# Kernel tuning notes

Hardware: AMD Instinct MI355X
Metric: run time of the kernel (lower is better)

## Reference

```python
import jax, jax.numpy as jnp
import numpy as np

N_HEADS = 8
OUT_DIM = 256   # node_dim + time_dim
KEY_DIM = 384   # node_dim + edge_dim + time_dim
HEAD_DIM = OUT_DIM // N_HEADS
LN_EPS = 1e-5


def setup_inputs() -> dict:
    key = jax.random.key(0)
    ks = jax.random.split(key, 12)
    B, N, D = 8192, 32, 128
    s = lambda fan_in: 1.0 / np.sqrt(fan_in)
    return {
        "node_feat": jax.random.normal(ks[0], (B, D), jnp.float32),
        "time_feat": jax.random.normal(ks[1], (B, D), jnp.float32),
        "edge_feat": jax.random.normal(ks[2], (B, N, D), jnp.float32),
        "nbr_node_feat": jax.random.normal(ks[3], (B, N, D), jnp.float32),
        "nbr_time_feat": jax.random.normal(ks[4], (B, N, D), jnp.float32),
        "nbr_mask": jax.random.randint(ks[5], (B, N), 0, 2, jnp.int64),
        # parameters, stored as [in, out] so y = x @ W
        "W_Q": jax.random.uniform(ks[6], (OUT_DIM, OUT_DIM), jnp.float32, -s(OUT_DIM), s(OUT_DIM)),
        "W_KV": jax.random.uniform(ks[7], (KEY_DIM, 2 * OUT_DIM), jnp.float32, -s(KEY_DIM), s(KEY_DIM)),
        "W_O": jax.random.uniform(ks[8], (OUT_DIM, OUT_DIM), jnp.float32, -s(OUT_DIM), s(OUT_DIM)),
        "b_O": jax.random.uniform(ks[9], (OUT_DIM,), jnp.float32, -s(OUT_DIM), s(OUT_DIM)),
        "ln_gamma": jnp.ones((OUT_DIM,), jnp.float32),
        "ln_beta": jnp.zeros((OUT_DIM,), jnp.float32),
    }


def reference(node_feat, time_feat, edge_feat, nbr_node_feat, nbr_time_feat,
              nbr_mask, W_Q, W_KV, W_O, b_O, ln_gamma, ln_beta):
    B = node_feat.shape[0]
    # query/residual: [B, out_dim] (query length is 1)
    R = jnp.concatenate([node_feat, time_feat], axis=1)
    Q = (R @ W_Q).reshape(B, N_HEADS, HEAD_DIM)                    # [B,H,d]
    Z = jnp.concatenate([nbr_node_feat, edge_feat, nbr_time_feat], axis=-1) @ W_KV  # [B,N,2*out]
    K = Z[:, :, :OUT_DIM].reshape(B, -1, N_HEADS, HEAD_DIM)        # [B,N,H,d]
    V = Z[:, :, OUT_DIM:].reshape(B, -1, N_HEADS, HEAD_DIM)
    A = jnp.einsum("bhd,bnhd->bhn", Q, K) * (HEAD_DIM ** -0.5)    # [B,H,N]
    masked = (nbr_mask == 0)[:, None, :]                           # [B,1,N]
    A = jnp.where(masked, jnp.float32(-1e10), A)
    A = jax.nn.softmax(A, axis=-1)                                 # dropout is identity (eval / p used at inference off)
    O = jnp.einsum("bhn,bnhd->bhd", A, V).reshape(B, OUT_DIM)
    out = O @ W_O + b_O
    x = out + R
    mu = jnp.mean(x, axis=-1, keepdims=True)
    var = jnp.mean(jnp.square(x - mu), axis=-1, keepdims=True)
    return (x - mu) * jax.lax.rsqrt(var + LN_EPS) * ln_gamma + ln_beta
```

## Files before the change

### kernel.cpp

```cpp
#include <hip/hip_runtime.h>

typedef __attribute__((ext_vector_type(8))) short bf16x8;
typedef __attribute__((ext_vector_type(4))) float f32x4;

#define MSTRIDE 264
#define XSTRIDE 392

__device__ __align__(16) unsigned short g_WQT[256 * 256];
__device__ __align__(16) unsigned short g_WKVT[512 * 384];
__device__ __align__(16) unsigned short g_WOT[256 * 256];

__device__ __forceinline__ float b2f(unsigned short u) {
    union { unsigned int i; float f; } v; v.i = ((unsigned int)u) << 16; return v.f;
}
__device__ __forceinline__ unsigned short f2b(float f) {
    union { float f; unsigned int i; } v; v.f = f;
    unsigned int x = v.i;
    return (unsigned short)((x + 0x7fffu + ((x >> 16) & 1u)) >> 16);
}

__global__ void transcvt(const float* __restrict__ src, unsigned short* __restrict__ dst,
                         int R, int C) {
    __shared__ float tile[32][33];
    const int c0 = blockIdx.x * 32, r0 = blockIdx.y * 32;
    const int tx = threadIdx.x, ty = threadIdx.y;
#pragma unroll
    for (int i = 0; i < 32; i += 8)
        tile[ty + i][tx] = src[(size_t)(r0 + ty + i) * C + (c0 + tx)];
    __syncthreads();
#pragma unroll
    for (int i = 0; i < 32; i += 8)
        dst[(size_t)(c0 + ty + i) * R + (r0 + tx)] = f2b(tile[tx][ty + i]);
}

__device__ __forceinline__ void ld8f(const float* __restrict__ s, unsigned short* dst) {
    const float4 a = *(const float4*)s;
    const float4 b = *(const float4*)(s + 4);
    unsigned short t[8];
    t[0] = f2b(a.x); t[1] = f2b(a.y); t[2] = f2b(a.z); t[3] = f2b(a.w);
    t[4] = f2b(b.x); t[5] = f2b(b.y); t[6] = f2b(b.z); t[7] = f2b(b.w);
    *(uint4*)dst = *(const uint4*)t;
}

__global__ __launch_bounds__(256, 2) void ta_fused(
    const float* __restrict__ node,
    const float* __restrict__ timef,
    const float* __restrict__ edge,
    const float* __restrict__ nbrnode,
    const float* __restrict__ nbrtime,
    const int* __restrict__ nmask,
    const float* __restrict__ bO,
    const float* __restrict__ gam,
    const float* __restrict__ bet,
    float* __restrict__ out)
{
    __shared__ __align__(16) unsigned short Xs[64 * XSTRIDE];
    __shared__ __align__(16) unsigned short Rb[16 * MSTRIDE];
    __shared__ __align__(16) unsigned short Ob[16 * MSTRIDE];
    __shared__ float lnb[2][256];
    __shared__ int   mk[2][32];

    const int gb0  = blockIdx.x * 2;
    const int tid  = threadIdx.x;
    const int w    = tid >> 6;
    const int lane = tid & 63;
    const int l15  = lane & 15;
    const int quad = lane >> 4;

    bool m64 = true;
    for (int i = 1; i < 64; i += 2) m64 = m64 && (nmask[i] == 0);

    {
        unsigned int* pO = (unsigned int*)Ob;
        for (int i = tid; i < 16 * MSTRIDE / 2; i += 256) pO[i] = 0u;
        unsigned int* pR = (unsigned int*)Rb;
        for (int i = tid + MSTRIDE; i < 16 * MSTRIDE / 2; i += 256) pR[i] = 0u;
    }
    if (tid < 64) {
        const int b = tid >> 5, s = tid & 31;
        if (s < 16) ld8f(node  + (size_t)(gb0 + b) * 128 + s * 8,        &Rb[b * MSTRIDE + s * 8]);
        else        ld8f(timef + (size_t)(gb0 + b) * 128 + (s - 16) * 8, &Rb[b * MSTRIDE + s * 8]);
    } else if (tid < 128) {
        const int t = tid - 64, b = t >> 5, n = t & 31;
        const size_t j = (size_t)(gb0 + b) * 32 + n;
        mk[b][n] = m64 ? nmask[2 * j] : nmask[j];
    }
#pragma unroll
    for (int i = 0; i < 12; i++) {
        const int g  = i * 256 + tid;
        const int r  = g / 48, c8 = g % 48;
        const float* base; int koff;
        if (c8 < 16)      { base = nbrnode; koff = c8 * 8; }
        else if (c8 < 32) { base = edge;    koff = (c8 - 16) * 8; }
        else              { base = nbrtime; koff = (c8 - 32) * 8; }
        ld8f(base + (size_t)(gb0 * 32 + r) * 128 + koff, &Xs[r * XSTRIDE + c8 * 8]);
    }
    __syncthreads();

    const f32x4 zero4 = {0.0f, 0.0f, 0.0f, 0.0f};

    f32x4 accq[4];
#pragma unroll
    for (int ct = 0; ct < 4; ct++) accq[ct] = zero4;
    {
        const unsigned short* wq = g_WQT + (size_t)(w * 64 + l15) * 256 + quad * 8;
#pragma unroll 2
        for (int kc = 0; kc < 8; kc++) {
            const bf16x8 afr = *(const bf16x8*)(&Rb[l15 * MSTRIDE + kc * 32 + quad * 8]);
#pragma unroll
            for (int ct = 0; ct < 4; ct++) {
                const bf16x8 b = *(const bf16x8*)(wq + (size_t)(ct * 16) * 256 + kc * 32);
                accq[ct] = __builtin_amdgcn_mfma_f32_16x16x32_bf16(afr, b, accq[ct], 0, 0, 0);
            }
        }
    }

    f32x4 accK[4][4], accV[4][4];
#pragma unroll
    for (int rt = 0; rt < 4; rt++)
#pragma unroll
        for (int ct = 0; ct < 4; ct++) { accK[rt][ct] = zero4; accV[rt][ct] = zero4; }
    {
        const unsigned short* wkv = g_WKVT + (size_t)(w * 64 + l15) * 384 + quad * 8;
#pragma unroll 2
        for (int kc = 0; kc < 12; kc++) {
            bf16x8 af[4];
#pragma unroll
            for (int rt = 0; rt < 4; rt++)
                af[rt] = *(const bf16x8*)(&Xs[(rt * 16 + l15) * XSTRIDE + kc * 32 + quad * 8]);
            bf16x8 bK[4], bV[4];
#pragma unroll
            for (int ct = 0; ct < 4; ct++) {
                bK[ct] = *(const bf16x8*)(wkv + (size_t)(ct * 16) * 384 + kc * 32);
                bV[ct] = *(const bf16x8*)(wkv + (size_t)(256 + ct * 16) * 384 + kc * 32);
            }
            __builtin_amdgcn_s_setprio(1);
#pragma unroll
            for (int ct = 0; ct < 4; ct++)
#pragma unroll
                for (int rt = 0; rt < 4; rt++) {
                    accK[rt][ct] = __builtin_amdgcn_mfma_f32_16x16x32_bf16(af[rt], bK[ct], accK[rt][ct], 0, 0, 0);
                    accV[rt][ct] = __builtin_amdgcn_mfma_f32_16x16x32_bf16(af[rt], bV[ct], accV[rt][ct], 0, 0, 0);
                }
            __builtin_amdgcn_s_setprio(0);
        }
    }

    float aw[2][2][2][4];
    const float scl = 0.17677669529663687f;
#pragma unroll
    for (int bb = 0; bb < 2; bb++) {
        float qv[4];
#pragma unroll
        for (int ct = 0; ct < 4; ct++) qv[ct] = __shfl(accq[ct][bb], l15, 64);
#pragma unroll
        for (int hl = 0; hl < 2; hl++) {
            float sv[2][4];
#pragma unroll
            for (int rtl = 0; rtl < 2; rtl++) {
                const int rt = bb * 2 + rtl;
#pragma unroll
                for (int rg = 0; rg < 4; rg++)
                    sv[rtl][rg] = accK[rt][2 * hl][rg] * qv[2 * hl]
                                + accK[rt][2 * hl + 1][rg] * qv[2 * hl + 1];
            }
#pragma unroll
            for (int m = 1; m <= 8; m <<= 1)
#pragma unroll
                for (int rtl = 0; rtl < 2; rtl++)
#pragma unroll
                    for (int rg = 0; rg < 4; rg++)
                        sv[rtl][rg] += __shfl_xor(sv[rtl][rg], m, 64);
            float mx = -3.0e38f;
#pragma unroll
            for (int rtl = 0; rtl < 2; rtl++)
#pragma unroll
                for (int rg = 0; rg < 4; rg++) {
                    const int n = rtl * 16 + quad * 4 + rg;
                    sv[rtl][rg] = (mk[bb][n] != 0) ? sv[rtl][rg] * scl : -1.0e10f;
                    mx = fmaxf(mx, sv[rtl][rg]);
                }
            mx = fmaxf(mx, __shfl_xor(mx, 16, 64));
            mx = fmaxf(mx, __shfl_xor(mx, 32, 64));
            float sum = 0.0f;
#pragma unroll
            for (int rtl = 0; rtl < 2; rtl++)
#pragma unroll
                for (int rg = 0; rg < 4; rg++) {
                    const float e = __expf(sv[rtl][rg] - mx);
                    aw[bb][hl][rtl][rg] = e;
                    sum += e;
                }
            sum += __shfl_xor(sum, 16, 64);
            sum += __shfl_xor(sum, 32, 64);
            const float inv = 1.0f / sum;
#pragma unroll
            for (int rtl = 0; rtl < 2; rtl++)
#pragma unroll
                for (int rg = 0; rg < 4; rg++)
                    aw[bb][hl][rtl][rg] *= inv;
        }
    }

#pragma unroll
    for (int bb = 0; bb < 2; bb++)
#pragma unroll
        for (int hl = 0; hl < 2; hl++)
#pragma unroll
            for (int ctl = 0; ctl < 2; ctl++) {
                const int ct = hl * 2 + ctl;
                float o = 0.0f;
#pragma unroll
                for (int rtl = 0; rtl < 2; rtl++)
#pragma unroll
                    for (int rg = 0; rg < 4; rg++)
                        o += aw[bb][hl][rtl][rg] * accV[bb * 2 + rtl][ct][rg];
                o += __shfl_xor(o, 16, 64);
                o += __shfl_xor(o, 32, 64);
                if (quad == 0) {
                    const int col = (w * 2 + hl) * 32 + ctl * 16 + l15;
                    Ob[bb * MSTRIDE + col] = f2b(o);
                }
            }
    __syncthreads();

    f32x4 acco[4];
#pragma unroll
    for (int ct = 0; ct < 4; ct++) acco[ct] = zero4;
    {
        const unsigned short* wo = g_WOT + (size_t)(w * 64 + l15) * 256 + quad * 8;
#pragma unroll 2
        for (int kc = 0; kc < 8; kc++) {
            const bf16x8 afr = *(const bf16x8*)(&Ob[l15 * MSTRIDE + kc * 32 + quad * 8]);
#pragma unroll
            for (int ct = 0; ct < 4; ct++) {
                const bf16x8 b = *(const bf16x8*)(wo + (size_t)(ct * 16) * 256 + kc * 32);
                acco[ct] = __builtin_amdgcn_mfma_f32_16x16x32_bf16(afr, b, acco[ct], 0, 0, 0);
            }
        }
    }
    if (quad == 0) {
#pragma unroll
        for (int ct = 0; ct < 4; ct++) {
#pragma unroll
            for (int r = 0; r < 2; r++) {
                const int col = w * 64 + ct * 16 + l15;
                lnb[r][col] = acco[ct][r] + bO[col] + b2f(Rb[r * MSTRIDE + col]);
            }
        }
    }
    __syncthreads();

    if (w < 2) {
        const int bb = w;
        float x[4]; float s = 0.0f;
#pragma unroll
        for (int i = 0; i < 4; i++) { x[i] = lnb[bb][lane + i * 64]; s += x[i]; }
#pragma unroll
        for (int m = 1; m <= 32; m <<= 1) s += __shfl_xor(s, m, 64);
        const float mu = s * (1.0f / 256.0f);
        float s2 = 0.0f;
#pragma unroll
        for (int i = 0; i < 4; i++) { const float d = x[i] - mu; s2 += d * d; }
#pragma unroll
        for (int m = 1; m <= 32; m <<= 1) s2 += __shfl_xor(s2, m, 64);
        const float rstd = rsqrtf(s2 * (1.0f / 256.0f) + 1e-5f);
#pragma unroll
        for (int i = 0; i < 4; i++) {
            const int col = lane + i * 64;
            out[(size_t)(gb0 + bb) * 256 + col] =
                (x[i] - mu) * rstd * gam[col] + bet[col];
        }
    }
}

extern "C" void kernel_launch(void* const* d_in, const int* in_sizes, int n_in,
                              void* d_out, int out_size, void* d_ws, size_t ws_size,
                              hipStream_t stream) {
    const float* node    = (const float*)d_in[0];
    const float* timef   = (const float*)d_in[1];
    const float* edge    = (const float*)d_in[2];
    const float* nbrnode = (const float*)d_in[3];
    const float* nbrtime = (const float*)d_in[4];
    const int*   nmask   = (const int*)d_in[5];
    const float* W_Q     = (const float*)d_in[6];
    const float* W_KV    = (const float*)d_in[7];
    const float* W_O     = (const float*)d_in[8];
    const float* bO      = (const float*)d_in[9];
    const float* gam     = (const float*)d_in[10];
    const float* bet     = (const float*)d_in[11];

    unsigned short *wqt, *wkvt, *wot;
    hipGetSymbolAddress((void**)&wqt,  HIP_SYMBOL(g_WQT));
    hipGetSymbolAddress((void**)&wkvt, HIP_SYMBOL(g_WKVT));
    hipGetSymbolAddress((void**)&wot,  HIP_SYMBOL(g_WOT));

    transcvt<<<dim3(8, 8),   dim3(32, 8), 0, stream>>>(W_Q,  wqt,  256, 256);
    transcvt<<<dim3(16, 12), dim3(32, 8), 0, stream>>>(W_KV, wkvt, 384, 512);
    transcvt<<<dim3(8, 8),   dim3(32, 8), 0, stream>>>(W_O,  wot,  256, 256);

    ta_fused<<<4096, 256, 0, stream>>>(node, timef, edge, nbrnode, nbrtime, nmask,
                                       bO, gam, bet, (float*)d_out);
}
```

Measured before the change: 682.2 us.

## Software-pipeline weight and activation loads in fused attention GEMMs, merge weight conversion

Each GEMM loop (Q, KV, O projections) now double-buffers its weight and LDS fragments, prefetching the next k-chunk while MFMAs run, and the first weight fragments are issued before the barrier. Q values go to shared memory instead of being kept live through the KV loop, and the mask check uses an OR reduction. The three weight transpose-convert launches are merged into one. Register pressure rises from the extra buffers under launch_bounds(256,2), which could cause spills.

```diff
diff --git a/kernel.cpp b/kernel.cpp
--- a/kernel.cpp
+++ b/kernel.cpp
@@ -19,10 +19,17 @@
     return (unsigned short)((x + 0x7fffu + ((x >> 16) & 1u)) >> 16);
 }
 
-__global__ void transcvt(const float* __restrict__ src, unsigned short* __restrict__ dst,
-                         int R, int C) {
+__global__ void transcvt_all(const float* __restrict__ wq, const float* __restrict__ wkv,
+                             const float* __restrict__ wo,
+                             unsigned short* __restrict__ dq, unsigned short* __restrict__ dkv,
+                             unsigned short* __restrict__ dwo) {
     __shared__ float tile[32][33];
-    const int c0 = blockIdx.x * 32, r0 = blockIdx.y * 32;
+    const int b = blockIdx.x;
+    const float* src; unsigned short* dst; int R, C, bx, by;
+    if (b < 64)       { src = wq;  dst = dq;  R = 256; C = 256; bx = b & 7;  by = b >> 3; }
+    else if (b < 256) { const int t = b - 64;  src = wkv; dst = dkv; R = 384; C = 512; bx = t & 15; by = t >> 4; }
+    else              { const int t = b - 256; src = wo;  dst = dwo; R = 256; C = 256; bx = t & 7;  by = t >> 3; }
+    const int c0 = bx * 32, r0 = by * 32;
     const int tx = threadIdx.x, ty = threadIdx.y;
 #pragma unroll
     for (int i = 0; i < 32; i += 8)
@@ -57,6 +64,7 @@
     __shared__ __align__(16) unsigned short Xs[64 * XSTRIDE];
     __shared__ __align__(16) unsigned short Rb[16 * MSTRIDE];
     __shared__ __align__(16) unsigned short Ob[16 * MSTRIDE];
+    __shared__ float Qs[2][256];
     __shared__ float lnb[2][256];
     __shared__ int   mk[2][32];
 
@@ -67,8 +75,10 @@
     const int l15  = lane & 15;
     const int quad = lane >> 4;
 
-    bool m64 = true;
-    for (int i = 1; i < 64; i += 2) m64 = m64 && (nmask[i] == 0);
+    int orv = 0;
+#pragma unroll
+    for (int i = 1; i < 64; i += 2) orv |= nmask[i];
+    const bool m64 = (orv == 0);
 
     {
         unsigned int* pO = (unsigned int*)Ob;
@@ -95,6 +105,22 @@
         else              { base = nbrtime; koff = (c8 - 32) * 8; }
         ld8f(base + (size_t)(gb0 * 32 + r) * 128 + koff, &Xs[r * XSTRIDE + c8 * 8]);
     }
+
+    const unsigned short* wq  = g_WQT  + (size_t)(w * 64 + l15) * 256 + quad * 8;
+    const unsigned short* wkv = g_WKVT + (size_t)(w * 64 + l15) * 384 + quad * 8;
+    const unsigned short* wo  = g_WOT  + (size_t)(w * 64 + l15) * 256 + quad * 8;
+    bf16x8 bq[2][4], bK[2][4], bV[2][4];
+#pragma unroll
+    for (int p = 0; p < 2; p++)
+#pragma unroll
+        for (int ct = 0; ct < 4; ct++)
+            bq[p][ct] = *(const bf16x8*)(wq + (size_t)(ct * 16) * 256 + p * 32);
+#pragma unroll
+    for (int ct = 0; ct < 4; ct++) {
+        bK[0][ct] = *(const bf16x8*)(wkv + (size_t)(ct * 16) * 384);
+        bV[0][ct] = *(const bf16x8*)(wkv + (size_t)(256 + ct * 16) * 384);
+    }
+
     __syncthreads();
 
     const f32x4 zero4 = {0.0f, 0.0f, 0.0f, 0.0f};
@@ -103,15 +129,28 @@
 #pragma unroll
     for (int ct = 0; ct < 4; ct++) accq[ct] = zero4;
     {
-        const unsigned short* wq = g_WQT + (size_t)(w * 64 + l15) * 256 + quad * 8;
-#pragma unroll 2
+        bf16x8 aq[2];
+        aq[0] = *(const bf16x8*)(&Rb[l15 * MSTRIDE + 0 * 32 + quad * 8]);
+        aq[1] = *(const bf16x8*)(&Rb[l15 * MSTRIDE + 1 * 32 + quad * 8]);
+#pragma unroll
         for (int kc = 0; kc < 8; kc++) {
-            const bf16x8 afr = *(const bf16x8*)(&Rb[l15 * MSTRIDE + kc * 32 + quad * 8]);
-#pragma unroll
-            for (int ct = 0; ct < 4; ct++) {
-                const bf16x8 b = *(const bf16x8*)(wq + (size_t)(ct * 16) * 256 + kc * 32);
-                accq[ct] = __builtin_amdgcn_mfma_f32_16x16x32_bf16(afr, b, accq[ct], 0, 0, 0);
-            }
+            const int s = kc & 1;
+#pragma unroll
+            for (int ct = 0; ct < 4; ct++)
+                accq[ct] = __builtin_amdgcn_mfma_f32_16x16x32_bf16(aq[s], bq[s][ct], accq[ct], 0, 0, 0);
+            if (kc + 2 < 8) {
+                aq[s] = *(const bf16x8*)(&Rb[l15 * MSTRIDE + (kc + 2) * 32 + quad * 8]);
+#pragma unroll
+                for (int ct = 0; ct < 4; ct++)
+                    bq[s][ct] = *(const bf16x8*)(wq + (size_t)(ct * 16) * 256 + (kc + 2) * 32);
+            }
+        }
+    }
+    if (quad == 0) {
+#pragma unroll
+        for (int ct = 0; ct < 4; ct++) {
+            Qs[0][w * 64 + ct * 16 + l15] = accq[ct][0];
+            Qs[1][w * 64 + ct * 16 + l15] = accq[ct][1];
         }
     }
 
@@ -121,30 +160,48 @@
 #pragma unroll
         for (int ct = 0; ct < 4; ct++) { accK[rt][ct] = zero4; accV[rt][ct] = zero4; }
     {
-        const unsigned short* wkv = g_WKVT + (size_t)(w * 64 + l15) * 384 + quad * 8;
-#pragma unroll 2
+        bf16x8 af[2][4];
+#pragma unroll
+        for (int rt = 0; rt < 4; rt++)
+            af[0][rt] = *(const bf16x8*)(&Xs[(rt * 16 + l15) * XSTRIDE + quad * 8]);
+#pragma unroll
+        for (int ct = 0; ct < 4; ct++) {
+            bK[1][ct] = *(const bf16x8*)(wkv + (size_t)(ct * 16) * 384 + 32);
+            bV[1][ct] = *(const bf16x8*)(wkv + (size_t)(256 + ct * 16) * 384 + 32);
+        }
+#pragma unroll
         for (int kc = 0; kc < 12; kc++) {
-            bf16x8 af[4];
-#pragma unroll
-            for (int rt = 0; rt < 4; rt++)
-                af[rt] = *(const bf16x8*)(&Xs[(rt * 16 + l15) * XSTRIDE + kc * 32 + quad * 8]);
-            bf16x8 bK[4], bV[4];
-#pragma unroll
-            for (int ct = 0; ct < 4; ct++) {
-                bK[ct] = *(const bf16x8*)(wkv + (size_t)(ct * 16) * 384 + kc * 32);
-                bV[ct] = *(const bf16x8*)(wkv + (size_t)(256 + ct * 16) * 384 + kc * 32);
+            const int s = kc & 1;
+            if (kc + 1 < 12) {
+#pragma unroll
+                for (int rt = 0; rt < 4; rt++)
+                    af[s ^ 1][rt] = *(const bf16x8*)(&Xs[(rt * 16 + l15) * XSTRIDE + (kc + 1) * 32 + quad * 8]);
             }
             __builtin_amdgcn_s_setprio(1);
 #pragma unroll
             for (int ct = 0; ct < 4; ct++)
 #pragma unroll
                 for (int rt = 0; rt < 4; rt++) {
-                    accK[rt][ct] = __builtin_amdgcn_mfma_f32_16x16x32_bf16(af[rt], bK[ct], accK[rt][ct], 0, 0, 0);
-                    accV[rt][ct] = __builtin_amdgcn_mfma_f32_16x16x32_bf16(af[rt], bV[ct], accV[rt][ct], 0, 0, 0);
+                    accK[rt][ct] = __builtin_amdgcn_mfma_f32_16x16x32_bf16(af[s][rt], bK[s][ct], accK[rt][ct], 0, 0, 0);
+                    accV[rt][ct] = __builtin_amdgcn_mfma_f32_16x16x32_bf16(af[s][rt], bV[s][ct], accV[rt][ct], 0, 0, 0);
                 }
             __builtin_amdgcn_s_setprio(0);
-        }
-    }
+            if (kc + 2 < 12) {
+#pragma unroll
+                for (int ct = 0; ct < 4; ct++) {
+                    bK[s][ct] = *(const bf16x8*)(wkv + (size_t)(ct * 16) * 384 + (kc + 2) * 32);
+                    bV[s][ct] = *(const bf16x8*)(wkv + (size_t)(256 + ct * 16) * 384 + (kc + 2) * 32);
+                }
+            }
+        }
+    }
+
+    bf16x8 bo[2][4];
+#pragma unroll
+    for (int p = 0; p < 2; p++)
+#pragma unroll
+        for (int ct = 0; ct < 4; ct++)
+            bo[p][ct] = *(const bf16x8*)(wo + (size_t)(ct * 16) * 256 + p * 32);
 
     float aw[2][2][2][4];
     const float scl = 0.17677669529663687f;
@@ -152,7 +209,7 @@
     for (int bb = 0; bb < 2; bb++) {
         float qv[4];
 #pragma unroll
-        for (int ct = 0; ct < 4; ct++) qv[ct] = __shfl(accq[ct][bb], l15, 64);
+        for (int ct = 0; ct < 4; ct++) qv[ct] = Qs[bb][w * 64 + ct * 16 + l15];
 #pragma unroll
         for (int hl = 0; hl < 2; hl++) {
             float sv[2][4];
@@ -228,14 +285,20 @@
 #pragma unroll
     for (int ct = 0; ct < 4; ct++) acco[ct] = zero4;
     {
-        const unsigned short* wo = g_WOT + (size_t)(w * 64 + l15) * 256 + quad * 8;
-#pragma unroll 2
+        bf16x8 ao[2];
+        ao[0] = *(const bf16x8*)(&Ob[l15 * MSTRIDE + 0 * 32 + quad * 8]);
+        ao[1] = *(const bf16x8*)(&Ob[l15 * MSTRIDE + 1 * 32 + quad * 8]);
+#pragma unroll
         for (int kc = 0; kc < 8; kc++) {
-            const bf16x8 afr = *(const bf16x8*)(&Ob[l15 * MSTRIDE + kc * 32 + quad * 8]);
-#pragma unroll
-            for (int ct = 0; ct < 4; ct++) {
-                const bf16x8 b = *(const bf16x8*)(wo + (size_t)(ct * 16) * 256 + kc * 32);
-                acco[ct] = __builtin_amdgcn_mfma_f32_16x16x32_bf16(afr, b, acco[ct], 0, 0, 0);
+            const int s = kc & 1;
+#pragma unroll
+            for (int ct = 0; ct < 4; ct++)
+                acco[ct] = __builtin_amdgcn_mfma_f32_16x16x32_bf16(ao[s], bo[s][ct], acco[ct], 0, 0, 0);
+            if (kc + 2 < 8) {
+                ao[s] = *(const bf16x8*)(&Ob[l15 * MSTRIDE + (kc + 2) * 32 + quad * 8]);
+#pragma unroll
+                for (int ct = 0; ct < 4; ct++)
+                    bo[s][ct] = *(const bf16x8*)(wo + (size_t)(ct * 16) * 256 + (kc + 2) * 32);
             }
         }
     }
@@ -295,9 +358,7 @@
     hipGetSymbolAddress((void**)&wkvt, HIP_SYMBOL(g_WKVT));
     hipGetSymbolAddress((void**)&wot,  HIP_SYMBOL(g_WOT));
 
-    transcvt<<<dim3(8, 8),   dim3(32, 8), 0, stream>>>(W_Q,  wqt,  256, 256);
-    transcvt<<<dim3(16, 12), dim3(32, 8), 0, stream>>>(W_KV, wkvt, 384, 512);
-    transcvt<<<dim3(8, 8),   dim3(32, 8), 0, stream>>>(W_O,  wot,  256, 256);
+    transcvt_all<<<320, dim3(32, 8), 0, stream>>>(W_Q, W_KV, W_O, wqt, wkvt, wot);
 
     ta_fused<<<4096, 256, 0, stream>>>(node, timef, edge, nbrnode, nbrtime, nmask,
                                        bO, gam, bet, (float*)d_out);
```

Measured after the change: 666.0 us. 1.02x faster.
